# Kernel tuning notes

Measured on AMD Instinct MI355X. Metric: run time of the kernel, lower is better.

Reference implementation:

```python
import jax, jax.numpy as jnp
import numpy as np
from jax import lax
import math

SCALES = (128.0, 256.0, 512.0)
ASPECT_RATIOS = (0.5, 1.0, 2.0)
NMS_THR = 0.7
PRENMS_TOPK = 2000   # rpn_train_prenms_topk (module is in training mode at __init__)
POST_TOPK = 300      # rpn_train_topk
MIN_SIZE = 16.0      # rpn_min_size
BBOX_CLAMP = math.log(1000.0 / 16.0)


def conv2d(x, w, b, pad):
    y = lax.conv_general_dilated(x, w, (1, 1), pad,
                                 dimension_numbers=('NCHW', 'OIHW', 'NCHW'))
    return y + b[None, :, None, None]


def generate_anchors(img_h, img_w, grid_h, grid_w, dtype=jnp.float32):
    # Mirrors RegionProposalNetwork.generate_anchors
    stride_h = img_h // grid_h
    stride_w = img_w // grid_w
    scales = jnp.asarray(SCALES, dtype)
    ratios = jnp.asarray(ASPECT_RATIOS, dtype)
    h = jnp.sqrt(ratios)
    w = 1.0 / h
    ws = (w[:, None] * scales[None, :]).reshape(-1)   # (K,)
    hs = (h[:, None] * scales[None, :]).reshape(-1)
    base = jnp.round(jnp.stack([-ws, -hs, ws, hs], axis=1) / 2.0)  # (K,4)
    sx = jnp.arange(grid_w, dtype=dtype) * stride_w
    sy = jnp.arange(grid_h, dtype=dtype) * stride_h
    syy, sxx = jnp.meshgrid(sy, sx, indexing='ij')
    sxx = sxx.reshape(-1); syy = syy.reshape(-1)
    shifts = jnp.stack([sxx, syy, sxx, syy], axis=1)               # (HW,4)
    anchors = (shifts[:, None, :] + base[None, :, :]).reshape(-1, 4)  # (HW*K,4)
    return anchors


def decode(deltas, anchors):
    wa = anchors[:, 2] - anchors[:, 0]
    ha = anchors[:, 3] - anchors[:, 1]
    cxa = anchors[:, 0] + 0.5 * wa
    cya = anchors[:, 1] + 0.5 * ha
    dx, dy = deltas[..., 0], deltas[..., 1]
    dw = jnp.minimum(deltas[..., 2], BBOX_CLAMP)
    dh = jnp.minimum(deltas[..., 3], BBOX_CLAMP)
    cx = dx * wa + cxa
    cy = dy * ha + cya
    w = jnp.exp(dw) * wa
    h = jnp.exp(dh) * ha
    return jnp.stack([cx - 0.5 * w, cy - 0.5 * h, cx + 0.5 * w, cy + 0.5 * h], axis=-1)


def pairwise_iou(a, b):
    area_a = (a[:, 2] - a[:, 0]) * (a[:, 3] - a[:, 1])
    area_b = (b[:, 2] - b[:, 0]) * (b[:, 3] - b[:, 1])
    lt = jnp.maximum(a[:, None, :2], b[None, :, :2])
    rb = jnp.minimum(a[:, None, 2:], b[None, :, 2:])
    wh = jnp.clip(rb - lt, 0.0)
    inter = wh[..., 0] * wh[..., 1]
    return inter / (area_a[:, None] + area_b[None, :] - inter)


def nms_keep(boxes, init_suppressed):
    # boxes are already sorted by descending score; O(N^2) matrix NMS.
    iou = lax.stop_gradient(pairwise_iou(boxes, boxes))
    n = boxes.shape[0]
    idxs = jnp.arange(n)
    def body(i, st):
        keep, sup = st
        valid = jnp.logical_not(sup[i])
        keep = keep.at[i].set(valid)
        sup = sup | (valid & (iou[i] > NMS_THR) & (idxs > i))
        return keep, sup
    keep, _ = lax.fori_loop(0, n, body,
                            (jnp.zeros(n, dtype=bool), init_suppressed))
    return keep


def filter_one(proposals, scores, img_h, img_w):
    # pre-NMS top-k
    sc, idx = lax.top_k(scores, PRENMS_TOPK)
    boxes = proposals[idx]
    # clip to image
    x1 = jnp.clip(boxes[:, 0], 0.0, img_w)
    y1 = jnp.clip(boxes[:, 1], 0.0, img_h)
    x2 = jnp.clip(boxes[:, 2], 0.0, img_w)
    y2 = jnp.clip(boxes[:, 3], 0.0, img_h)
    boxes = jnp.stack([x1, y1, x2, y2], axis=1)
    # min-size filter (masked, fixed shape)
    small = ((x2 - x1) < MIN_SIZE) | ((y2 - y1) < MIN_SIZE)
    sc = jnp.where(small, -jnp.inf, sc)
    # NMS then post-NMS top-k
    keep = nms_keep(boxes, small)
    post = jnp.where(keep, sc, -jnp.inf)
    fs, fi = lax.top_k(post, POST_TOPK)
    return boxes[fi], fs


def setup_inputs() -> dict:
    key = jax.random.key(0)
    ks = jax.random.split(key, 8)
    B, C, H, W, IMG, K = 4, 512, 64, 64, 1024, 9
    image = jax.random.normal(ks[0], (B, 3, IMG, IMG), jnp.float32)
    feature_map = jax.random.normal(ks[1], (B, C, H, W), jnp.float32)
    # init: normal(std=0.01) weights, zero bias
    w_conv = 0.01 * jax.random.normal(ks[2], (C, C, 3, 3), jnp.float32)
    b_conv = jnp.zeros((C,), jnp.float32)
    w_cls = 0.01 * jax.random.normal(ks[3], (K, C, 1, 1), jnp.float32)
    b_cls = jnp.zeros((K,), jnp.float32)
    w_box = 0.01 * jax.random.normal(ks[4], (4 * K, C, 1, 1), jnp.float32)
    b_box = jnp.zeros((4 * K,), jnp.float32)
    return {"image": image, "feature_map": feature_map,
            "w_conv": w_conv, "b_conv": b_conv,
            "w_cls": w_cls, "b_cls": b_cls,
            "w_box": w_box, "b_box": b_box}


def reference(image, feature_map, w_conv, b_conv, w_cls, b_cls, w_box, b_box):
    B, _, img_h, img_w = image.shape
    _, _, gh, gw = feature_map.shape
    feat = jax.nn.relu(conv2d(feature_map, w_conv, b_conv, 'SAME'))
    cls = conv2d(feat, w_cls, b_cls, 'VALID')   # (B, K, H, W)
    box = conv2d(feat, w_box, b_box, 'VALID')   # (B, 4K, H, W)
    scores = jax.nn.sigmoid(cls.transpose(0, 2, 3, 1).reshape(B, -1))   # (B, N)
    deltas = box.transpose(0, 2, 3, 1).reshape(B, -1, 4)                # (B, N, 4)
    anchors = generate_anchors(img_h, img_w, gh, gw)                    # (N, 4)
    proposals = decode(deltas, anchors)                                 # (B, N, 4)
    props, sc = jax.vmap(lambda p, s: filter_one(p, s, float(img_h), float(img_w)))(proposals, scores)
    return props, sc   # (B, POST_TOPK, 4), (B, POST_TOPK)
```

## Files before the change

### kernel.cpp

```cpp
#include <hip/hip_runtime.h>
#include <math.h>

typedef unsigned long long U64;
typedef _Float16 half8 __attribute__((ext_vector_type(8)));
typedef float f32x16 __attribute__((ext_vector_type(16)));

__device__ const float g_bw[9] = {91.f, 181.f, 362.f, 64.f, 128.f, 256.f, 45.f, 91.f, 181.f};
__device__ const float g_bh[9] = {45.f, 91.f, 181.f, 64.f, 128.f, 256.f, 91.f, 181.f, 362.f};

__device__ inline f32x16 zero16() {
    f32x16 z;
#pragma unroll
    for (int i = 0; i < 16; ++i) z[i] = 0.f;
    return z;
}

__global__ __launch_bounds__(256) void k_prep_fm(const float* __restrict__ fm,
                                                 _Float16* __restrict__ fph,
                                                 _Float16* __restrict__ fpl) {
    __shared__ float tile[64][65];
    int cg = blockIdx.x, h = blockIdx.y, b = blockIdx.z;
    int t = threadIdx.x;
    int cl = t >> 2, w0 = (t & 3) * 16;
    const float* src = fm + (((size_t)(b * 512 + cg * 64 + cl) * 64 + h) * 64 + w0);
#pragma unroll
    for (int l = 0; l < 4; ++l) {
        float4 v = *(const float4*)(src + l * 4);
        tile[cl][w0 + l * 4 + 0] = v.x; tile[cl][w0 + l * 4 + 1] = v.y;
        tile[cl][w0 + l * 4 + 2] = v.z; tile[cl][w0 + l * 4 + 3] = v.w;
    }
    __syncthreads();
    int wI = t >> 2, c0l = (t & 3) * 16;
    size_t dst = ((size_t)(b * 66 + h + 1) * 66 + (wI + 1)) * 512 + cg * 64 + c0l;
#pragma unroll
    for (int pair = 0; pair < 2; ++pair) {
        half8 hv, lv;
#pragma unroll
        for (int i = 0; i < 8; ++i) {
            float x = tile[c0l + pair * 8 + i][wI];
            _Float16 hi = (_Float16)x;
            hv[i] = hi;
            lv[i] = (_Float16)((x - (float)hi) * 2048.0f);
        }
        *(half8*)(fph + dst + pair * 8) = hv;
        *(half8*)(fpl + dst + pair * 8) = lv;
    }
}

__global__ __launch_bounds__(256) void k_prep_w(const float* __restrict__ w_conv,
                                                _Float16* __restrict__ wkh,
                                                _Float16* __restrict__ wkl) {
    __shared__ float wb[4608];
    int o = blockIdx.x, t = threadIdx.x;
    for (int e = t; e < 4608; e += 256) wb[e] = w_conv[(size_t)o * 4608 + e];
    __syncthreads();
    for (int e = t; e < 4608; e += 256) {
        int c = e & 511, r = e >> 9;
        float x = wb[c * 9 + r];
        _Float16 hi = (_Float16)x;
        wkh[(size_t)o * 4608 + e] = hi;
        wkl[(size_t)o * 4608 + e] = (_Float16)((x - (float)hi) * 2048.0f);
    }
}

__global__ __launch_bounds__(256, 2) void k_conv_mfma(
    const _Float16* __restrict__ fph, const _Float16* __restrict__ fpl,
    const _Float16* __restrict__ wkh, const _Float16* __restrict__ wkl,
    const float* __restrict__ bconv, float* __restrict__ feat) {
    __shared__ _Float16 As[2][128][64];
    __shared__ _Float16 Bs[2][128][64];
    const int t = threadIdx.x;
    const int lane = t & 63, wv = t >> 6;
    const int wm = wv >> 1, wn = wv & 1;
    const int p0 = blockIdx.x * 128, o0 = blockIdx.y * 128;

    const int srow = t >> 2;
    const int scol = (t & 3) * 8;
    int idxA[2], idxB[2], woff[2][2];
#pragma unroll
    for (int h2 = 0; h2 < 2; ++h2) {
        int r = h2 * 64 + srow;
        int P = p0 + r;
        int bb = P >> 12, hh = (P >> 6) & 63, ww = P & 63;
        idxA[h2] = ((bb * 66 + hh) * 66 + ww) * 512 + scol;
        idxB[h2] = (o0 + r) * 4608 + scol;
        woff[h2][0] = r * 128 + ((((t & 3) + 0) * 16) ^ ((r & 7) << 4));
        woff[h2][1] = r * 128 + ((((t & 3) + 4) * 16) ^ ((r & 7) << 4));
    }

    f32x16 acc0[2][2], acc1[2][2];
#pragma unroll
    for (int mi = 0; mi < 2; ++mi)
#pragma unroll
        for (int ni = 0; ni < 2; ++ni) { acc0[mi][ni] = zero16(); acc1[mi][ni] = zero16(); }

    half8 sa[2][2], sb[2][2];
    auto stage = [&](int k0) {
        int rr = k0 >> 9, c0 = k0 & 511;
        int ry = (rr * 11) >> 5, rx = rr - ry * 3;
        int koffA = (ry * 66 + rx) * 512 + c0;
#pragma unroll
        for (int h2 = 0; h2 < 2; ++h2) {
            sa[h2][0] = *(const half8*)(fph + idxA[h2] + koffA);
            sa[h2][1] = *(const half8*)(fpl + idxA[h2] + koffA);
            sb[h2][0] = *(const half8*)(wkh + idxB[h2] + k0);
            sb[h2][1] = *(const half8*)(wkl + idxB[h2] + k0);
        }
    };
    auto commit = [&](int buf) {
        char* ab = (char*)As + buf * 16384;
        char* bb = (char*)Bs + buf * 16384;
#pragma unroll
        for (int h2 = 0; h2 < 2; ++h2) {
            *(half8*)(ab + woff[h2][0]) = sa[h2][0];
            *(half8*)(ab + woff[h2][1]) = sa[h2][1];
            *(half8*)(bb + woff[h2][0]) = sb[h2][0];
            *(half8*)(bb + woff[h2][1]) = sb[h2][1];
        }
    };

    stage(0);
    commit(0);
    __syncthreads();

    for (int it = 0; it < 144; ++it) {
        int cur = it & 1;
        if (it < 143) stage((it + 1) * 32);
        const char* ab = (const char*)As + cur * 16384;
        const char* bb = (const char*)Bs + cur * 16384;
        half8 af[2][2][2], bf[2][2][2];
        const int lg = (lane >> 5) * 16;
#pragma unroll
        for (int mi = 0; mi < 2; ++mi) {
            int rA = wm * 64 + mi * 32 + (lane & 31);
            int xa = (rA & 7) << 4, ba = rA * 128;
#pragma unroll
            for (int hl = 0; hl < 2; ++hl)
#pragma unroll
                for (int kh = 0; kh < 2; ++kh)
                    af[mi][hl][kh] = *(const half8*)(ab + ba + ((hl * 64 + kh * 32 + lg) ^ xa));
        }
#pragma unroll
        for (int ni = 0; ni < 2; ++ni) {
            int rB = wn * 64 + ni * 32 + (lane & 31);
            int xb = (rB & 7) << 4, bb0 = rB * 128;
#pragma unroll
            for (int hl = 0; hl < 2; ++hl)
#pragma unroll
                for (int kh = 0; kh < 2; ++kh)
                    bf[ni][hl][kh] = *(const half8*)(bb + bb0 + ((hl * 64 + kh * 32 + lg) ^ xb));
        }
#pragma unroll
        for (int mi = 0; mi < 2; ++mi)
#pragma unroll
            for (int ni = 0; ni < 2; ++ni) {
                acc0[mi][ni] = __builtin_amdgcn_mfma_f32_32x32x16_f16(af[mi][0][0], bf[ni][0][0], acc0[mi][ni], 0, 0, 0);
                acc0[mi][ni] = __builtin_amdgcn_mfma_f32_32x32x16_f16(af[mi][0][1], bf[ni][0][1], acc0[mi][ni], 0, 0, 0);
                acc1[mi][ni] = __builtin_amdgcn_mfma_f32_32x32x16_f16(af[mi][0][0], bf[ni][1][0], acc1[mi][ni], 0, 0, 0);
                acc1[mi][ni] = __builtin_amdgcn_mfma_f32_32x32x16_f16(af[mi][0][1], bf[ni][1][1], acc1[mi][ni], 0, 0, 0);
                acc1[mi][ni] = __builtin_amdgcn_mfma_f32_32x32x16_f16(af[mi][1][0], bf[ni][0][0], acc1[mi][ni], 0, 0, 0);
                acc1[mi][ni] = __builtin_amdgcn_mfma_f32_32x32x16_f16(af[mi][1][1], bf[ni][0][1], acc1[mi][ni], 0, 0, 0);
            }
        if (it < 143) commit(cur ^ 1);
        __syncthreads();
    }

#pragma unroll
    for (int mi = 0; mi < 2; ++mi)
#pragma unroll
        for (int ni = 0; ni < 2; ++ni) {
            int col = o0 + wn * 64 + ni * 32 + (lane & 31);
            float bv = bconv[col];
            int rbase = p0 + wm * 64 + mi * 32 + 4 * (lane >> 5);
#pragma unroll
            for (int q = 0; q < 16; ++q) {
                int row = rbase + (q & 3) + 8 * (q >> 2);
                float v = acc0[mi][ni][q] + acc1[mi][ni][q] * 4.8828125e-4f + bv;
                feat[(size_t)row * 512 + col] = fmaxf(v, 0.f);
            }
        }
}

__global__ __launch_bounds__(256) void k_heads(const float* __restrict__ feat,
                                               const float* __restrict__ w_cls,
                                               const float* __restrict__ b_cls,
                                               const float* __restrict__ w_box,
                                               const float* __restrict__ b_box,
                                               float* __restrict__ scores,
                                               float* __restrict__ deltas) {
    __shared__ float red[3][64][45];
    int t = threadIdx.x;
    int px = t & 63, cq = t >> 6;
    int p = blockIdx.x * 64 + px;
    const float* fr = feat + (size_t)p * 512 + cq * 128;
    float acc[45];
#pragma unroll
    for (int o = 0; o < 45; ++o) acc[o] = 0.f;
    for (int c = 0; c < 128; c += 4) {
        float4 f = *(const float4*)(fr + c);
#pragma unroll
        for (int o = 0; o < 45; ++o) {
            const float* wr = ((o < 9) ? (w_cls + o * 512) : (w_box + (o - 9) * 512)) + cq * 128 + c;
            acc[o] += f.x * wr[0] + f.y * wr[1] + f.z * wr[2] + f.w * wr[3];
        }
    }
    if (cq > 0) {
#pragma unroll
        for (int o = 0; o < 45; ++o) red[cq - 1][px][o] = acc[o];
    }
    __syncthreads();
    if (cq == 0) {
#pragma unroll
        for (int o = 0; o < 45; ++o) acc[o] += red[0][px][o] + red[1][px][o] + red[2][px][o];
        int b = p >> 12, pixloc = p & 4095;
        int sbase = b * 36864 + pixloc * 9;
#pragma unroll
        for (int o = 0; o < 9; ++o) {
            float x = acc[o] + b_cls[o];
            scores[sbase + o] = 1.f / (1.f + expf(-x));
        }
#pragma unroll
        for (int c36 = 0; c36 < 36; ++c36) {
            float x = acc[9 + c36] + b_box[c36];
            int a = c36 >> 2, comp = c36 & 3;
            deltas[(size_t)(sbase + a) * 4 + comp] = x;
        }
    }
}

__global__ __launch_bounds__(256) void k_decode_keys(const float* __restrict__ scores,
                                                     const float* __restrict__ deltas,
                                                     U64* __restrict__ keys,
                                                     float4* __restrict__ proposals) {
    int i = blockIdx.x * 256 + threadIdx.x;
    int b = blockIdx.y;
    float s = scores[b * 36864 + i];
    keys[b * 36864 + i] =
        (((U64)(__float_as_uint(s) ^ 0x80000000u)) << 32) | (unsigned)(~(unsigned)i);
    int pix = i / 9;
    int a = i - pix * 9;
    int h = pix >> 6, w = pix & 63;
    float bw = g_bw[a], bh = g_bh[a];
    float cxa = (float)(w * 16), cya = (float)(h * 16);
    float wa = 2.f * bw, ha = 2.f * bh;
    const float4 d = *(const float4*)(deltas + (size_t)(b * 36864 + i) * 4);
    float dw = fminf(d.z, 4.135166556742356f);
    float dh = fminf(d.w, 4.135166556742356f);
    float cx = d.x * wa + cxa;
    float cy = d.y * ha + cya;
    float pw = expf(dw) * wa;
    float ph = expf(dh) * ha;
    proposals[b * 36864 + i] =
        make_float4(cx - 0.5f * pw, cy - 0.5f * ph, cx + 0.5f * pw, cy + 0.5f * ph);
}

__device__ inline void cmp_stage(U64* s, int j, int k, int tid) {
    for (int p = tid; p < 1024; p += 256) {
        int il = ((p & ~(j - 1)) << 1) | (p & (j - 1));
        int ip = il | j;
        U64 a = s[il], c = s[ip];
        bool desc = ((il & k) == 0);
        bool sw = desc ? (a < c) : (a > c);
        if (sw) { s[il] = c; s[ip] = a; }
    }
}

__global__ __launch_bounds__(256) void k_sort_chunk(const U64* __restrict__ keys,
                                                    U64* __restrict__ run) {
    __shared__ U64 s[2048];
    int b = blockIdx.x / 18, ch = blockIdx.x % 18;
    int tid = threadIdx.x;
    const U64* src = keys + (size_t)b * 36864 + ch * 2048;
    for (int e = tid; e < 2048; e += 256) s[e] = src[e];
    __syncthreads();
    for (int k = 2; k <= 2048; k <<= 1)
        for (int j = k >> 1; j >= 1; j >>= 1) {
            cmp_stage(s, j, k, tid);
            __syncthreads();
        }
    U64* dst = run + ((size_t)b * 18 + ch) * 2048;
    for (int e = tid; e < 2048; e += 256) dst[e] = s[e];
}

__global__ __launch_bounds__(256) void k_merge(const U64* __restrict__ in,
                                               U64* __restrict__ out, int nc) {
    __shared__ U64 s[4096];
    int j = blockIdx.x, b = blockIdx.y;
    int tid = threadIdx.x;
    const U64* A = in + ((size_t)b * 18 + 2 * j) * 2048;
    U64* O = out + ((size_t)b * 18 + j) * 2048;
    if (2 * j + 1 < nc) {
        const U64* Bp = in + ((size_t)b * 18 + 2 * j + 1) * 2048;
        for (int e = tid; e < 2048; e += 256) { s[e] = A[e]; s[4095 - e] = Bp[e]; }
        __syncthreads();
        for (int jj = 2048; jj >= 1; jj >>= 1) {
            for (int p = tid; p < 2048; p += 256) {
                int il = ((p & ~(jj - 1)) << 1) | (p & (jj - 1));
                int ip = il | jj;
                U64 a = s[il], c = s[ip];
                if (a < c) { s[il] = c; s[ip] = a; }
            }
            __syncthreads();
        }
        for (int e = tid; e < 2048; e += 256) O[e] = s[e];
    } else {
        for (int e = tid; e < 2048; e += 256) O[e] = A[e];
    }
}

__global__ __launch_bounds__(256) void k_topk_gather(const U64* __restrict__ runf,
                                                     const float4* __restrict__ proposals,
                                                     float4* __restrict__ tb_boxes,
                                                     float* __restrict__ tb_scores) {
    int g = blockIdx.x * 256 + threadIdx.x;
    if (g >= 8000) return;
    int b = g / 2000, r = g - b * 2000;
    U64 key = runf[(size_t)b * 18 * 2048 + r];
    unsigned n = ~((unsigned)key);
    float s = __uint_as_float(((unsigned)(key >> 32)) ^ 0x80000000u);
    float4 p = proposals[b * 36864 + (int)n];
    float x1 = fminf(fmaxf(p.x, 0.f), 1024.f);
    float y1 = fminf(fmaxf(p.y, 0.f), 1024.f);
    float x2 = fminf(fmaxf(p.z, 0.f), 1024.f);
    float y2 = fminf(fmaxf(p.w, 0.f), 1024.f);
    bool small_ = ((x2 - x1) < 16.f) || ((y2 - y1) < 16.f);
    tb_boxes[g] = make_float4(x1, y1, x2, y2);
    tb_scores[g] = small_ ? -INFINITY : s;
}

__global__ __launch_bounds__(64) void k_nms_mask(const float4* __restrict__ tb_boxes,
                                                 U64* __restrict__ mask) {
    int jt = blockIdx.x, it = blockIdx.y, b = blockIdx.z;
    int tid = threadIdx.x;
    __shared__ float4 jb[64];
    int j0 = jt * 64;
    {
        int j = j0 + tid;
        jb[tid] = (j < 2000) ? tb_boxes[b * 2000 + j] : make_float4(0.f, 0.f, 0.f, 0.f);
    }
    __syncthreads();
    int i = it * 64 + tid;
    if (i >= 2000) return;
    float4 bi = tb_boxes[b * 2000 + i];
    float ai = (bi.z - bi.x) * (bi.w - bi.y);
    U64 bits = 0;
#pragma unroll 4
    for (int jj = 0; jj < 64; ++jj) {
        int j = j0 + jj;
        float4 bj = jb[jj];
        float aj = (bj.z - bj.x) * (bj.w - bj.y);
        float ltx = fmaxf(bi.x, bj.x), lty = fmaxf(bi.y, bj.y);
        float rbx = fminf(bi.z, bj.z), rby = fminf(bi.w, bj.w);
        float ww = fmaxf(rbx - ltx, 0.f), hh2 = fmaxf(rby - lty, 0.f);
        float inter = ww * hh2;
        float iou = inter / (ai + aj - inter);
        if ((j > i) && (j < 2000) && (iou > 0.7f)) bits |= (1ull << jj);
    }
    mask[((size_t)b * 2000 + i) * 32 + jt] = bits;
}

__global__ __launch_bounds__(64) void k_nms_scan(const float4* __restrict__ tb_boxes,
                                                 const float* __restrict__ tb_scores,
                                                 const U64* __restrict__ mask,
                                                 float* __restrict__ out) {
    int b = blockIdx.x;
    int lane = threadIdx.x;
    __shared__ U64 mbuf[2][2048];
    __shared__ unsigned short keeplist[2000];
    __shared__ unsigned char keepflag[2000];
    __shared__ unsigned short fillq[304];

    U64 remv = 0;
    if (lane < 32) {
        for (int jj = 0; jj < 64; ++jj) {
            int j = (lane << 6) | jj;
            if (j < 2000 && tb_scores[b * 2000 + j] == -INFINITY) remv |= (1ull << jj);
        }
    }
    const U64* mb = mask + (size_t)b * 2000 * 32;
#pragma unroll
    for (int q = 0; q < 32; ++q) {
        int e = q * 64 + lane;
        mbuf[0][e] = mb[(e >> 5) * 32 + (e & 31)];
    }
    __syncthreads();

    int nkeep = 0;
    for (int ch = 0; ch < 32; ++ch) {
        int cur = ch & 1;
        U64 v[32];
        if (ch < 31) {
#pragma unroll
            for (int q = 0; q < 32; ++q) {
                int e = q * 64 + lane;
                int row = (ch + 1) * 64 + (e >> 5), wd = e & 31;
                v[q] = (row < 2000) ? mb[(size_t)row * 32 + wd] : 0ull;
            }
        }
        int iend = min(64, 2000 - ch * 64);
        U64 w_all = __shfl(remv, ch);
        for (int ii = 0; ii < iend; ++ii) {
            bool sup = (w_all >> ii) & 1ull;
            int i = ch * 64 + ii;
            if (!sup) {
                if (lane == 0) keeplist[nkeep] = (unsigned short)i;
                U64 mrow = mbuf[cur][(ii << 5) | (lane & 31)];
                if (lane < 32) remv |= mrow;
                w_all |= mbuf[cur][(ii << 5) | ch];
                nkeep++;
            }
            if (lane == 0) keepflag[i] = sup ? (unsigned char)0 : (unsigned char)1;
        }
        if (ch < 31) {
#pragma unroll
            for (int q = 0; q < 32; ++q) mbuf[cur ^ 1][q * 64 + lane] = v[q];
        }
        __syncthreads();
    }

    if (lane == 0) {
        int need = 300 - nkeep, c = 0;
        for (int i = 0; i < 2000 && c < need; ++i)
            if (!keepflag[i]) fillq[c++] = (unsigned short)i;
    }
    __syncthreads();
    for (int r = lane; r < 300; r += 64) {
        int src; float sc;
        if (r < nkeep) { src = keeplist[r]; sc = tb_scores[b * 2000 + src]; }
        else           { src = fillq[r - nkeep]; sc = -INFINITY; }
        float4 bx = tb_boxes[b * 2000 + src];
        int ob = (b * 300 + r) * 4;
        out[ob + 0] = bx.x; out[ob + 1] = bx.y; out[ob + 2] = bx.z; out[ob + 3] = bx.w;
        out[4800 + b * 300 + r] = sc;
    }
}

extern "C" void kernel_launch(void* const* d_in, const int* in_sizes, int n_in,
                              void* d_out, int out_size, void* d_ws, size_t ws_size,
                              hipStream_t stream) {
    (void)in_sizes; (void)n_in; (void)out_size; (void)ws_size;
    const float* feature_map = (const float*)d_in[1];
    const float* w_conv = (const float*)d_in[2];
    const float* b_conv = (const float*)d_in[3];
    const float* w_cls  = (const float*)d_in[4];
    const float* b_cls  = (const float*)d_in[5];
    const float* w_box  = (const float*)d_in[6];
    const float* b_box  = (const float*)d_in[7];
    float* out = (float*)d_out;

    char* ws = (char*)d_ws;
    size_t off = 0;
    auto alloc = [&](size_t bytes) {
        void* p = ws + off;
        off = (off + bytes + 255) & ~(size_t)255;
        return p;
    };
    const size_t fp_elems = 4ull * 66 * 66 * 512;
    _Float16* fph = (_Float16*)alloc(fp_elems * 2);
    _Float16* fpl = (_Float16*)alloc(fp_elems * 2);
    _Float16* wkh = (_Float16*)alloc(512ull * 4608 * 2);
    _Float16* wkl = (_Float16*)alloc(512ull * 4608 * 2);
    float*  feat      = (float*) alloc(16384ull * 512 * 4);
    float*  scores    = (float*) alloc(4ull * 36864 * 4);
    float*  deltas    = (float*) alloc(4ull * 36864 * 4 * 4);
    float4* proposals = (float4*)alloc(4ull * 36864 * 16);
    U64*    keys      = (U64*)   alloc(4ull * 36864 * 8);
    U64*    run0      = (U64*)   alloc(4ull * 18 * 2048 * 8);
    U64*    run1      = (U64*)   alloc(4ull * 18 * 2048 * 8);
    float4* tb_boxes  = (float4*)alloc(8000ull * 16);
    float*  tb_scores = (float*) alloc(8000ull * 4);
    U64*    nmsmask   = (U64*)   alloc(8000ull * 32 * 8);

    hipMemsetAsync(fph, 0, fp_elems * 2, stream);
    hipMemsetAsync(fpl, 0, fp_elems * 2, stream);
    k_prep_fm<<<dim3(8, 64, 4), 256, 0, stream>>>(feature_map, fph, fpl);
    k_prep_w<<<512, 256, 0, stream>>>(w_conv, wkh, wkl);
    k_conv_mfma<<<dim3(128, 4), 256, 0, stream>>>(fph, fpl, wkh, wkl, b_conv, feat);
    k_heads<<<256, 256, 0, stream>>>(feat, w_cls, b_cls, w_box, b_box, scores, deltas);
    k_decode_keys<<<dim3(144, 4), 256, 0, stream>>>(scores, deltas, keys, proposals);

    k_sort_chunk<<<72, 256, 0, stream>>>(keys, run0);
    U64* bufs[2] = {run0, run1};
    int nc = 18, src = 0;
    while (nc > 1) {
        int nm = (nc + 1) / 2;
        k_merge<<<dim3(nm, 4), 256, 0, stream>>>(bufs[src], bufs[src ^ 1], nc);
        src ^= 1;
        nc = nm;
    }
    k_topk_gather<<<32, 256, 0, stream>>>(bufs[src], proposals, tb_boxes, tb_scores);
    k_nms_mask<<<dim3(32, 32, 4), 64, 0, stream>>>(tb_boxes, nmsmask);
    k_nms_scan<<<4, 64, 0, stream>>>(tb_boxes, tb_scores, nmsmask, out);
}
```

Baseline: 823.7 us.

## Use direct global-to-LDS loads in conv, fuse decode into heads, 4-way merges

The conv GEMM now loads its hi/lo fp16 operands from interleaved buffers straight into LDS through global_load_lds, with two tiles in flight, explicit vmcnt waits and a swizzled block order. This removes the register staging round-trip and is meant to improve L2 reuse. The heads kernel now writes sort keys and decoded proposals directly, which drops the separate decode kernel and the scores/deltas buffers. The pairwise merge passes become 4-way merges, cutting the number of kernel launches. The manual wait counts and LDS layout must stay consistent with the swizzled reads, or the conv results will be corrupted.

Measured after the change: 786.8 us. 1.05x faster.

```diff
diff --git a/kernel.cpp b/kernel.cpp
--- a/kernel.cpp
+++ b/kernel.cpp
@@ -15,9 +15,13 @@
     return z;
 }
 
+#define GLOAD16(G, L)                                                  \
+    __builtin_amdgcn_global_load_lds(                                  \
+        (const __attribute__((address_space(1))) void*)(G),            \
+        (__attribute__((address_space(3))) void*)(L), 16, 0, 0)
+
 __global__ __launch_bounds__(256) void k_prep_fm(const float* __restrict__ fm,
-                                                 _Float16* __restrict__ fph,
-                                                 _Float16* __restrict__ fpl) {
+                                                 _Float16* __restrict__ fpi) {
     __shared__ float tile[64][65];
     int cg = blockIdx.x, h = blockIdx.y, b = blockIdx.z;
     int t = threadIdx.x;
@@ -30,62 +34,61 @@
         tile[cl][w0 + l * 4 + 2] = v.z; tile[cl][w0 + l * 4 + 3] = v.w;
     }
     __syncthreads();
-    int wI = t >> 2, c0l = (t & 3) * 16;
-    size_t dst = ((size_t)(b * 66 + h + 1) * 66 + (wI + 1)) * 512 + cg * 64 + c0l;
-#pragma unroll
-    for (int pair = 0; pair < 2; ++pair) {
-        half8 hv, lv;
+    int w = t & 63, pth = t >> 6;
+    int chunkrel = pth >> 1, half = pth & 1;
+    _Float16* dst = fpi + ((size_t)((b * 66 + h + 1) * 66) + (w + 1)) * 1024 +
+                    (cg * 2 + chunkrel) * 64 + half * 32;
+#pragma unroll
+    for (int g8 = 0; g8 < 4; ++g8) {
+        half8 v;
 #pragma unroll
         for (int i = 0; i < 8; ++i) {
-            float x = tile[c0l + pair * 8 + i][wI];
+            float x = tile[chunkrel * 32 + g8 * 8 + i][w];
             _Float16 hi = (_Float16)x;
-            hv[i] = hi;
-            lv[i] = (_Float16)((x - (float)hi) * 2048.0f);
-        }
-        *(half8*)(fph + dst + pair * 8) = hv;
-        *(half8*)(fpl + dst + pair * 8) = lv;
+            v[i] = half ? (_Float16)((x - (float)hi) * 2048.0f) : hi;
+        }
+        *(half8*)(dst + g8 * 8) = v;
     }
 }
 
 __global__ __launch_bounds__(256) void k_prep_w(const float* __restrict__ w_conv,
-                                                _Float16* __restrict__ wkh,
-                                                _Float16* __restrict__ wkl) {
+                                                _Float16* __restrict__ wki) {
     __shared__ float wb[4608];
     int o = blockIdx.x, t = threadIdx.x;
     for (int e = t; e < 4608; e += 256) wb[e] = w_conv[(size_t)o * 4608 + e];
     __syncthreads();
-    for (int e = t; e < 4608; e += 256) {
-        int c = e & 511, r = e >> 9;
-        float x = wb[c * 9 + r];
+    for (int e = t; e < 9216; e += 256) {
+        int s = e & 63, chunk = e >> 6;
+        int tap = chunk >> 4, cgi = chunk & 15;
+        int c = cgi * 32 + (s & 31);
+        float x = wb[c * 9 + tap];
         _Float16 hi = (_Float16)x;
-        wkh[(size_t)o * 4608 + e] = hi;
-        wkl[(size_t)o * 4608 + e] = (_Float16)((x - (float)hi) * 2048.0f);
+        wki[(size_t)o * 9216 + e] = (s < 32) ? hi : (_Float16)((x - (float)hi) * 2048.0f);
     }
 }
 
 __global__ __launch_bounds__(256, 2) void k_conv_mfma(
-    const _Float16* __restrict__ fph, const _Float16* __restrict__ fpl,
-    const _Float16* __restrict__ wkh, const _Float16* __restrict__ wkl,
+    const _Float16* __restrict__ fpi, const _Float16* __restrict__ wki,
     const float* __restrict__ bconv, float* __restrict__ feat) {
     __shared__ _Float16 As[2][128][64];
     __shared__ _Float16 Bs[2][128][64];
     const int t = threadIdx.x;
     const int lane = t & 63, wv = t >> 6;
     const int wm = wv >> 1, wn = wv & 1;
-    const int p0 = blockIdx.x * 128, o0 = blockIdx.y * 128;
-
-    const int srow = t >> 2;
-    const int scol = (t & 3) * 8;
-    int idxA[2], idxB[2], woff[2][2];
-#pragma unroll
-    for (int h2 = 0; h2 < 2; ++h2) {
-        int r = h2 * 64 + srow;
-        int P = p0 + r;
+    int flat = (int)blockIdx.x + 128 * (int)blockIdx.y;
+    int fid = (flat & 7) * 64 + (flat >> 3);
+    const int p0 = (fid >> 2) * 128, o0 = (fid & 3) * 128;
+
+    const char* baseA[4];
+    const char* baseB[4];
+#pragma unroll
+    for (int q = 0; q < 4; ++q) {
+        int row = wv * 32 + q * 8 + (lane >> 3);
+        int qs = (lane & 7) ^ (row & 7);
+        int P = p0 + row;
         int bb = P >> 12, hh = (P >> 6) & 63, ww = P & 63;
-        idxA[h2] = ((bb * 66 + hh) * 66 + ww) * 512 + scol;
-        idxB[h2] = (o0 + r) * 4608 + scol;
-        woff[h2][0] = r * 128 + ((((t & 3) + 0) * 16) ^ ((r & 7) << 4));
-        woff[h2][1] = r * 128 + ((((t & 3) + 4) * 16) ^ ((r & 7) << 4));
+        baseA[q] = (const char*)fpi + ((size_t)((bb * 66 + hh) * 66 + ww)) * 2048 + qs * 16;
+        baseB[q] = (const char*)wki + (size_t)(o0 + row) * 18432 + qs * 16;
     }
 
     f32x16 acc0[2][2], acc1[2][2];
@@ -94,40 +97,30 @@
 #pragma unroll
         for (int ni = 0; ni < 2; ++ni) { acc0[mi][ni] = zero16(); acc1[mi][ni] = zero16(); }
 
-    half8 sa[2][2], sb[2][2];
-    auto stage = [&](int k0) {
-        int rr = k0 >> 9, c0 = k0 & 511;
-        int ry = (rr * 11) >> 5, rx = rr - ry * 3;
-        int koffA = (ry * 66 + rx) * 512 + c0;
-#pragma unroll
-        for (int h2 = 0; h2 < 2; ++h2) {
-            sa[h2][0] = *(const half8*)(fph + idxA[h2] + koffA);
-            sa[h2][1] = *(const half8*)(fpl + idxA[h2] + koffA);
-            sb[h2][0] = *(const half8*)(wkh + idxB[h2] + k0);
-            sb[h2][1] = *(const half8*)(wkl + idxB[h2] + k0);
+    auto issue = [&](int it2, int buf) {
+        int tap = it2 >> 4;
+        int ry = (tap * 11) >> 5, rx = tap - ry * 3;
+        int ka = (ry * 66 + rx) * 2048 + (it2 & 15) * 128;
+        int kb = it2 * 128;
+#pragma unroll
+        for (int q = 0; q < 4; ++q) {
+            GLOAD16(baseA[q] + ka, &As[buf][wv * 32 + q * 8][0]);
+            GLOAD16(baseB[q] + kb, &Bs[buf][wv * 32 + q * 8][0]);
         }
     };
-    auto commit = [&](int buf) {
-        char* ab = (char*)As + buf * 16384;
-        char* bb = (char*)Bs + buf * 16384;
-#pragma unroll
-        for (int h2 = 0; h2 < 2; ++h2) {
-            *(half8*)(ab + woff[h2][0]) = sa[h2][0];
-            *(half8*)(ab + woff[h2][1]) = sa[h2][1];
-            *(half8*)(bb + woff[h2][0]) = sb[h2][0];
-            *(half8*)(bb + woff[h2][1]) = sb[h2][1];
-        }
-    };
-
-    stage(0);
-    commit(0);
-    __syncthreads();
+
+    issue(0, 0);
+    issue(1, 1);
 
     for (int it = 0; it < 144; ++it) {
         int cur = it & 1;
-        if (it < 143) stage((it + 1) * 32);
+        if (it < 143) { asm volatile("s_waitcnt vmcnt(8)" ::: "memory"); }
+        else          { asm volatile("s_waitcnt vmcnt(0)" ::: "memory"); }
+        __builtin_amdgcn_s_barrier();
+        __builtin_amdgcn_sched_barrier(0);
+
         const char* ab = (const char*)As + cur * 16384;
-        const char* bb = (const char*)Bs + cur * 16384;
+        const char* bb2 = (const char*)Bs + cur * 16384;
         half8 af[2][2][2], bf[2][2][2];
         const int lg = (lane >> 5) * 16;
 #pragma unroll
@@ -148,7 +141,7 @@
             for (int hl = 0; hl < 2; ++hl)
 #pragma unroll
                 for (int kh = 0; kh < 2; ++kh)
-                    bf[ni][hl][kh] = *(const half8*)(bb + bb0 + ((hl * 64 + kh * 32 + lg) ^ xb));
+                    bf[ni][hl][kh] = *(const half8*)(bb2 + bb0 + ((hl * 64 + kh * 32 + lg) ^ xb));
         }
 #pragma unroll
         for (int mi = 0; mi < 2; ++mi)
@@ -161,8 +154,11 @@
                 acc1[mi][ni] = __builtin_amdgcn_mfma_f32_32x32x16_f16(af[mi][1][0], bf[ni][0][0], acc1[mi][ni], 0, 0, 0);
                 acc1[mi][ni] = __builtin_amdgcn_mfma_f32_32x32x16_f16(af[mi][1][1], bf[ni][0][1], acc1[mi][ni], 0, 0, 0);
             }
-        if (it < 143) commit(cur ^ 1);
-        __syncthreads();
+
+        __builtin_amdgcn_sched_barrier(0);
+        __builtin_amdgcn_s_barrier();
+        __builtin_amdgcn_sched_barrier(0);
+        if (it < 142) issue(it + 2, cur);
     }
 
 #pragma unroll
@@ -186,8 +182,8 @@
                                                const float* __restrict__ b_cls,
                                                const float* __restrict__ w_box,
                                                const float* __restrict__ b_box,
-                                               float* __restrict__ scores,
-                                               float* __restrict__ deltas) {
+                                               U64* __restrict__ keys,
+                                               float4* __restrict__ proposals) {
     __shared__ float red[3][64][45];
     int t = threadIdx.x;
     int px = t & 63, cq = t >> 6;
@@ -213,45 +209,27 @@
 #pragma unroll
         for (int o = 0; o < 45; ++o) acc[o] += red[0][px][o] + red[1][px][o] + red[2][px][o];
         int b = p >> 12, pixloc = p & 4095;
-        int sbase = b * 36864 + pixloc * 9;
-#pragma unroll
-        for (int o = 0; o < 9; ++o) {
-            float x = acc[o] + b_cls[o];
-            scores[sbase + o] = 1.f / (1.f + expf(-x));
-        }
-#pragma unroll
-        for (int c36 = 0; c36 < 36; ++c36) {
-            float x = acc[9 + c36] + b_box[c36];
-            int a = c36 >> 2, comp = c36 & 3;
-            deltas[(size_t)(sbase + a) * 4 + comp] = x;
-        }
-    }
-}
-
-__global__ __launch_bounds__(256) void k_decode_keys(const float* __restrict__ scores,
-                                                     const float* __restrict__ deltas,
-                                                     U64* __restrict__ keys,
-                                                     float4* __restrict__ proposals) {
-    int i = blockIdx.x * 256 + threadIdx.x;
-    int b = blockIdx.y;
-    float s = scores[b * 36864 + i];
-    keys[b * 36864 + i] =
-        (((U64)(__float_as_uint(s) ^ 0x80000000u)) << 32) | (unsigned)(~(unsigned)i);
-    int pix = i / 9;
-    int a = i - pix * 9;
-    int h = pix >> 6, w = pix & 63;
-    float bw = g_bw[a], bh = g_bh[a];
-    float cxa = (float)(w * 16), cya = (float)(h * 16);
-    float wa = 2.f * bw, ha = 2.f * bh;
-    const float4 d = *(const float4*)(deltas + (size_t)(b * 36864 + i) * 4);
-    float dw = fminf(d.z, 4.135166556742356f);
-    float dh = fminf(d.w, 4.135166556742356f);
-    float cx = d.x * wa + cxa;
-    float cy = d.y * ha + cya;
-    float pw = expf(dw) * wa;
-    float ph = expf(dh) * ha;
-    proposals[b * 36864 + i] =
-        make_float4(cx - 0.5f * pw, cy - 0.5f * ph, cx + 0.5f * pw, cy + 0.5f * ph);
+        int h = pixloc >> 6, w = pixloc & 63;
+        int ibase = b * 36864 + pixloc * 9;
+#pragma unroll
+        for (int a = 0; a < 9; ++a) {
+            float logit = acc[a] + b_cls[a];
+            float s = 1.f / (1.f + expf(-logit));
+            keys[ibase + a] = (((U64)(__float_as_uint(s) ^ 0x80000000u)) << 32) |
+                              (unsigned)(~(unsigned)(pixloc * 9 + a));
+            float dx = acc[9 + a * 4 + 0] + b_box[a * 4 + 0];
+            float dy = acc[9 + a * 4 + 1] + b_box[a * 4 + 1];
+            float dw = fminf(acc[9 + a * 4 + 2] + b_box[a * 4 + 2], 4.135166556742356f);
+            float dh = fminf(acc[9 + a * 4 + 3] + b_box[a * 4 + 3], 4.135166556742356f);
+            float wa = 2.f * g_bw[a], ha = 2.f * g_bh[a];
+            float cx = dx * wa + (float)(w * 16);
+            float cy = dy * ha + (float)(h * 16);
+            float pw = expf(dw) * wa;
+            float ph = expf(dh) * ha;
+            proposals[ibase + a] =
+                make_float4(cx - 0.5f * pw, cy - 0.5f * ph, cx + 0.5f * pw, cy + 0.5f * ph);
+        }
+    }
 }
 
 __device__ inline void cmp_stage(U64* s, int j, int k, int tid) {
@@ -282,30 +260,35 @@
     for (int e = tid; e < 2048; e += 256) dst[e] = s[e];
 }
 
-__global__ __launch_bounds__(256) void k_merge(const U64* __restrict__ in,
-                                               U64* __restrict__ out, int nc) {
+__global__ __launch_bounds__(256) void k_merge4(const U64* __restrict__ in,
+                                                U64* __restrict__ out, int nc) {
     __shared__ U64 s[4096];
-    int j = blockIdx.x, b = blockIdx.y;
+    int g = blockIdx.x, b = blockIdx.y;
     int tid = threadIdx.x;
-    const U64* A = in + ((size_t)b * 18 + 2 * j) * 2048;
-    U64* O = out + ((size_t)b * 18 + j) * 2048;
-    if (2 * j + 1 < nc) {
-        const U64* Bp = in + ((size_t)b * 18 + 2 * j + 1) * 2048;
-        for (int e = tid; e < 2048; e += 256) { s[e] = A[e]; s[4095 - e] = Bp[e]; }
+    int r0 = g * 4;
+    int n = nc - r0; if (n > 4) n = 4;
+    const U64* base = in + (size_t)b * 18 * 2048;
+    U64* O = out + ((size_t)b * 18 + g) * 2048;
+    for (int e = tid; e < 2048; e += 256) s[e] = base[(size_t)r0 * 2048 + e];
+    for (int m = 1; m < n; ++m) {
+        for (int e = tid; e < 2048; e += 256) s[4095 - e] = base[(size_t)(r0 + m) * 2048 + e];
         __syncthreads();
-        for (int jj = 2048; jj >= 1; jj >>= 1) {
-            for (int p = tid; p < 2048; p += 256) {
-                int il = ((p & ~(jj - 1)) << 1) | (p & (jj - 1));
-                int ip = il | jj;
+        for (int e = tid; e < 2048; e += 256) {
+            U64 a = s[e], c = s[e + 2048];
+            s[e] = (a >= c) ? a : c;
+        }
+        __syncthreads();
+        for (int j = 1024; j >= 1; j >>= 1) {
+            for (int p = tid; p < 1024; p += 256) {
+                int il = ((p & ~(j - 1)) << 1) | (p & (j - 1));
+                int ip = il | j;
                 U64 a = s[il], c = s[ip];
                 if (a < c) { s[il] = c; s[ip] = a; }
             }
             __syncthreads();
         }
-        for (int e = tid; e < 2048; e += 256) O[e] = s[e];
-    } else {
-        for (int e = tid; e < 2048; e += 256) O[e] = A[e];
-    }
+    }
+    for (int e = tid; e < 2048; e += 256) O[e] = s[e];
 }
 
 __global__ __launch_bounds__(256) void k_topk_gather(const U64* __restrict__ runf,
@@ -455,14 +438,10 @@
         off = (off + bytes + 255) & ~(size_t)255;
         return p;
     };
-    const size_t fp_elems = 4ull * 66 * 66 * 512;
-    _Float16* fph = (_Float16*)alloc(fp_elems * 2);
-    _Float16* fpl = (_Float16*)alloc(fp_elems * 2);
-    _Float16* wkh = (_Float16*)alloc(512ull * 4608 * 2);
-    _Float16* wkl = (_Float16*)alloc(512ull * 4608 * 2);
+    const size_t fpi_elems = 4ull * 66 * 66 * 1024;
+    _Float16* fpi = (_Float16*)alloc(fpi_elems * 2);
+    _Float16* wki = (_Float16*)alloc(512ull * 9216 * 2);
     float*  feat      = (float*) alloc(16384ull * 512 * 4);
-    float*  scores    = (float*) alloc(4ull * 36864 * 4);
-    float*  deltas    = (float*) alloc(4ull * 36864 * 4 * 4);
     float4* proposals = (float4*)alloc(4ull * 36864 * 16);
     U64*    keys      = (U64*)   alloc(4ull * 36864 * 8);
     U64*    run0      = (U64*)   alloc(4ull * 18 * 2048 * 8);
@@ -471,24 +450,18 @@
     float*  tb_scores = (float*) alloc(8000ull * 4);
     U64*    nmsmask   = (U64*)   alloc(8000ull * 32 * 8);
 
-    hipMemsetAsync(fph, 0, fp_elems * 2, stream);
-    hipMemsetAsync(fpl, 0, fp_elems * 2, stream);
-    k_prep_fm<<<dim3(8, 64, 4), 256, 0, stream>>>(feature_map, fph, fpl);
-    k_prep_w<<<512, 256, 0, stream>>>(w_conv, wkh, wkl);
-    k_conv_mfma<<<dim3(128, 4), 256, 0, stream>>>(fph, fpl, wkh, wkl, b_conv, feat);
-    k_heads<<<256, 256, 0, stream>>>(feat, w_cls, b_cls, w_box, b_box, scores, deltas);
-    k_decode_keys<<<dim3(144, 4), 256, 0, stream>>>(scores, deltas, keys, proposals);
+    hipMemsetAsync(fpi, 0, fpi_elems * 2, stream);
+    k_prep_fm<<<dim3(8, 64, 4), 256, 0, stream>>>(feature_map, fpi);
+    k_prep_w<<<512, 256, 0, stream>>>(w_conv, wki);
+    k_conv_mfma<<<dim3(128, 4), 256, 0, stream>>>(fpi, wki, b_conv, feat);
+    k_heads<<<256, 256, 0, stream>>>(feat, w_cls, b_cls, w_box, b_box, keys, proposals);
 
     k_sort_chunk<<<72, 256, 0, stream>>>(keys, run0);
-    U64* bufs[2] = {run0, run1};
-    int nc = 18, src = 0;
-    while (nc > 1) {
-        int nm = (nc + 1) / 2;
-        k_merge<<<dim3(nm, 4), 256, 0, stream>>>(bufs[src], bufs[src ^ 1], nc);
-        src ^= 1;
-        nc = nm;
-    }
-    k_topk_gather<<<32, 256, 0, stream>>>(bufs[src], proposals, tb_boxes, tb_scores);
+    k_merge4<<<dim3(5, 4), 256, 0, stream>>>(run0, run1, 18);
+    k_merge4<<<dim3(2, 4), 256, 0, stream>>>(run1, run0, 5);
+    k_merge4<<<dim3(1, 4), 256, 0, stream>>>(run0, run1, 2);
+
+    k_topk_gather<<<32, 256, 0, stream>>>(run1, proposals, tb_boxes, tb_scores);
     k_nms_mask<<<dim3(32, 32, 4), 64, 0, stream>>>(tb_boxes, nmsmask);
     k_nms_scan<<<4, 64, 0, stream>>>(tb_boxes, tb_scores, nmsmask, out);
 }
```
